# Kernel optimization log

Measured on AMD Instinct MI355X. Metric: run time of the kernel, lower is better.

The kernel has to match this reference:

```python
import jax, jax.numpy as jnp
import numpy as np

N_NODES = 100000
N_EDGES = 3200000
N_GRAPHS = 256
FEAT = 128
HIDDEN = 128
N_CLASSES = 10


def setup_inputs() -> dict:
    key = jax.random.key(0)
    ks = jax.random.split(key, 12)
    x = jax.random.normal(ks[0], (N_NODES, FEAT), dtype=jnp.float32)
    edge_index = jax.random.randint(ks[1], (2, N_EDGES), 0, N_NODES, dtype=jnp.int64)
    batch = jnp.sort(jax.random.randint(ks[2], (N_NODES,), 0, N_GRAPHS, dtype=jnp.int64))
    s = 0.05
    return {
        "x": x,
        "edge_index": edge_index,
        "batch": batch,
        "W1": jax.random.normal(ks[3], (FEAT, HIDDEN), dtype=jnp.float32) * s,
        "b1": jnp.zeros((HIDDEN,), dtype=jnp.float32),
        "W2": jax.random.normal(ks[4], (HIDDEN, HIDDEN), dtype=jnp.float32) * s,
        "b2": jnp.zeros((HIDDEN,), dtype=jnp.float32),
        "W3": jax.random.normal(ks[5], (HIDDEN, HIDDEN), dtype=jnp.float32) * s,
        "b3": jnp.zeros((HIDDEN,), dtype=jnp.float32),
        "lin1_w": jax.random.normal(ks[6], (HIDDEN, HIDDEN), dtype=jnp.float32) * s,
        "lin1_b": jnp.zeros((HIDDEN,), dtype=jnp.float32),
        "lin2_w": jax.random.normal(ks[7], (HIDDEN, N_CLASSES), dtype=jnp.float32) * s,
        "lin2_b": jnp.zeros((N_CLASSES,), dtype=jnp.float32),
    }


def _gcn_norm(edge_index, n_nodes):
    # PyG GCNConv default: add self-loops, symmetric normalization.
    src = jnp.concatenate([edge_index[0], jnp.arange(n_nodes, dtype=edge_index.dtype)])
    dst = jnp.concatenate([edge_index[1], jnp.arange(n_nodes, dtype=edge_index.dtype)])
    deg = jax.ops.segment_sum(jnp.ones_like(dst, dtype=jnp.float32), dst, num_segments=n_nodes)
    dis = jnp.where(deg > 0, jax.lax.rsqrt(jnp.maximum(deg, 1.0)), 0.0)
    norm = dis[src] * dis[dst]  # [E + N]
    return src, dst, norm


def _gcn_conv(x, src, dst, norm, W, b, n_nodes):
    h = x @ W                               # [N, H]
    msg = h[src] * norm[:, None]            # gather + scale, [E+N, H]
    out = jax.ops.segment_sum(msg, dst, num_segments=n_nodes)  # scatter-add
    return out + b


def reference(x, edge_index, batch, W1, b1, W2, b2, W3, b3, lin1_w, lin1_b, lin2_w, lin2_b):
    n = x.shape[0]
    src, dst, norm = _gcn_norm(edge_index, n)
    h = jax.nn.relu(_gcn_conv(x, src, dst, norm, W1, b1, n))
    h = jax.nn.relu(_gcn_conv(h, src, dst, norm, W2, b2, n))
    h = jax.nn.relu(_gcn_conv(h, src, dst, norm, W3, b3, n))
    # global mean pool over graphs
    sums = jax.ops.segment_sum(h, batch, num_segments=N_GRAPHS)
    cnts = jax.ops.segment_sum(jnp.ones((n,), dtype=h.dtype), batch, num_segments=N_GRAPHS)
    g = sums / jnp.maximum(cnts, 1.0)[:, None]
    g = jax.nn.relu(g @ lin1_w + lin1_b)
    # dropout p=0.5 is identity at inference
    return g @ lin2_w + lin2_b
```

## Files before the change

### kernel.cpp

```cpp
#include <hip/hip_runtime.h>
#include <hip/hip_fp16.h>

#define FEAT 128
#define CHUNK 8192
#define BSH 7
#define CAP 6144
#define RSTRIDE 784

#define QS  16.0f
#define QSI 0.0625f

typedef _Float16 half8 __attribute__((ext_vector_type(8)));
typedef float floatx4 __attribute__((ext_vector_type(4)));
typedef float floatx2 __attribute__((ext_vector_type(2)));

__device__ __forceinline__ unsigned int enc8x4(float a, float b, float c, float d) {
  unsigned int r = __builtin_amdgcn_cvt_pk_fp8_f32(a, b, 0u, false);
  return __builtin_amdgcn_cvt_pk_fp8_f32(c, d, r, true);
}
__device__ __forceinline__ void acc8(unsigned int w, float* a) {
  floatx2 v0 = __builtin_amdgcn_cvt_pk_f32_fp8(w, false);
  floatx2 v1 = __builtin_amdgcn_cvt_pk_f32_fp8(w, true);
  a[0] += v0.x; a[1] += v0.y; a[2] += v1.x; a[3] += v1.y;
}
__device__ __forceinline__ void acc8s(unsigned int w, float s, float* a) {
  floatx2 v0 = __builtin_amdgcn_cvt_pk_f32_fp8(w, false);
  floatx2 v1 = __builtin_amdgcn_cvt_pk_f32_fp8(w, true);
  a[0] = fmaf(s, v0.x, a[0]); a[1] = fmaf(s, v0.y, a[1]);
  a[2] = fmaf(s, v1.x, a[2]); a[3] = fmaf(s, v1.y, a[3]);
}


__global__ __launch_bounds__(256) void sort_prep_kernel(
    const int* __restrict__ ei, int E, int nchunks, int nbuk,
    int* __restrict__ pairs, int* __restrict__ runs,
    const float* __restrict__ W1, const float* __restrict__ W2,
    const float* __restrict__ W3, _Float16* __restrict__ P1,
    _Float16* __restrict__ P2, _Float16* __restrict__ P3,
    unsigned char* __restrict__ qA, unsigned char* __restrict__ qB,
    float* __restrict__ dis, float* __restrict__ gsum, int G, int N) {
  __shared__ int lhist[1024];
  __shared__ int lofs[1024];
  __shared__ int lcur[1024];
  __shared__ int tsum[256];
  __shared__ int stage[CHUNK];
  int t = threadIdx.x;
  if ((int)blockIdx.x >= nchunks) {
    int b = blockIdx.x - nchunks;
    if (b == 24) {
      if (t < 16) ((unsigned long long*)(qA + (size_t)N * FEAT))[t] = 0ull;
      else if (t < 32) ((unsigned long long*)(qB + (size_t)N * FEAT))[t - 16] = 0ull;
      else if (t == 32) dis[N] = 0.f;
      return;
    }
    if (b == 25) {
      float4 z = {0.f, 0.f, 0.f, 0.f};
      for (int i = t; i < G * 32; i += 256) ((float4*)gsum)[i] = z;
      return;
    }
    const float* W = (b < 8) ? W1 : (b < 16) ? W2 : W3;
    _Float16* P = (b < 8) ? P1 : (b < 16) ? P2 : P3;
    int e = (b & 7) * 256 + t;
    int l = e & 63;
    int ks = (e >> 6) & 3;
    int tn = e >> 8;
    int n = tn * 16 + (l & 15);
    int k0 = ks * 32 + (l >> 4) * 8;
    half8 v;
#pragma unroll
    for (int j = 0; j < 8; ++j) v[j] = (_Float16)W[(k0 + j) * 128 + n];
    *(half8*)(P + (size_t)e * 8) = v;
    return;
  }
  int c = blockIdx.x;
  int e0 = c * CHUNK;
  int e1 = e0 + CHUNK; if (e1 > E) e1 = E;
  int cnt = e1 - e0;
#pragma unroll
  for (int u = 0; u < 4; ++u) lhist[t + u * 256] = 0;
  __syncthreads();
  for (int j = e0 + t; j < e1; j += 256) atomicAdd(&lhist[ei[E + j] >> BSH], 1);
  __syncthreads();
  int a0 = lhist[4 * t], a1 = lhist[4 * t + 1];
  int a2 = lhist[4 * t + 2], a3 = lhist[4 * t + 3];
  int s = ((a0 + a1) + (a2 + a3));
  tsum[t] = s;
  __syncthreads();
  for (int o = 1; o < 256; o <<= 1) {
    int x = (t >= o) ? tsum[t - o] : 0;
    __syncthreads();
    tsum[t] += x;
    __syncthreads();
  }
  int base = tsum[t] - s;
  lofs[4 * t] = base;       lcur[4 * t] = base;
  lofs[4 * t + 1] = base + a0;           lcur[4 * t + 1] = base + a0;
  lofs[4 * t + 2] = base + a0 + a1;      lcur[4 * t + 2] = base + a0 + a1;
  lofs[4 * t + 3] = base + a0 + a1 + a2; lcur[4 * t + 3] = base + a0 + a1 + a2;
  __syncthreads();
  for (int k = t; k < nbuk; k += 256) runs[(size_t)c * RSTRIDE + k] = lofs[k];
  if (t == 0) runs[(size_t)c * RSTRIDE + nbuk] = cnt;
  for (int j = e0 + t; j < e1; j += 256) {
    int sv = ei[j];
    int d = ei[E + j];
    int p = atomicAdd(&lcur[d >> BSH], 1);
    stage[p] = sv | ((d & 127) << 24);
  }
  __syncthreads();
  for (int j = t; j < cnt; j += 256) pairs[e0 + j] = stage[j];
}

__global__ __launch_bounds__(256) void csr_mm1_kernel(
    const int* __restrict__ pairs, const int* __restrict__ runs, int nchunks,
    int nbuk, int2* __restrict__ row_se, float* __restrict__ dis,
    int* __restrict__ col,
    const float* __restrict__ Av, const _Float16* __restrict__ Wpk,
    unsigned char* __restrict__ qA, int N) {
  __shared__ int rs[512], rl[512], ro[512];
  __shared__ int cnt[128], sc[128];
  __shared__ int stage[CAP];
  int t = threadIdx.x;
  if ((int)blockIdx.x >= nbuk) {
    int wave = t >> 6, lane = t & 63;
    int quad = lane >> 4, nidx = lane & 15;
    int m0 = (blockIdx.x - nbuk) * 64 + wave * 16;
    int arow = m0 + nidx;
    bool avalid = arow < N;
    floatx4 acc[8];
#pragma unroll
    for (int tn = 0; tn < 8; ++tn) acc[tn] = (floatx4){0.f, 0.f, 0.f, 0.f};
#pragma unroll
    for (int ks = 0; ks < 4; ++ks) {
      half8 x = {};
      if (avalid) {
        const float* p = Av + (size_t)arow * 128 + ks * 32 + quad * 8;
        float4 f0 = *(const float4*)p;
        float4 f1 = *(const float4*)(p + 4);
        x[0] = (_Float16)f0.x; x[1] = (_Float16)f0.y;
        x[2] = (_Float16)f0.z; x[3] = (_Float16)f0.w;
        x[4] = (_Float16)f1.x; x[5] = (_Float16)f1.y;
        x[6] = (_Float16)f1.z; x[7] = (_Float16)f1.w;
      }
#pragma unroll
      for (int tn = 0; tn < 8; ++tn) {
        half8 wfrag = *(const half8*)(Wpk + ((size_t)((tn * 4 + ks) * 64 + lane)) * 8);
        acc[tn] = __builtin_amdgcn_mfma_f32_16x16x32_f16(wfrag, x, acc[tn], 0, 0, 0);
      }
    }
    if (avalid) {
#pragma unroll
      for (int tn = 0; tn < 8; ++tn) {
        unsigned int r = enc8x4(acc[tn][0] * QS, acc[tn][1] * QS,
                                acc[tn][2] * QS, acc[tn][3] * QS);
        *(unsigned int*)(qA + (size_t)arow * 128 + tn * 16 + quad * 4) = r;
      }
    }
    return;
  }
  int b = blockIdx.x;
  for (int c = t; c < 512; c += 256) {
    int s0 = 0, len = 0;
    if (c < nchunks) {
      const int* rr = runs + (size_t)c * RSTRIDE;
      s0 = rr[b];
      len = rr[b + 1] - s0;
    }
    rs[c] = s0; rl[c] = len;
  }
  if (t < 128) cnt[t] = 0;
  __syncthreads();
  ro[t] = rl[t]; ro[t + 256] = rl[t + 256];
  __syncthreads();
  for (int o = 1; o < 512; o <<= 1) {
    int v0 = (t >= o) ? ro[t - o] : 0;
    int v1 = (t + 256 >= o) ? ro[t + 256 - o] : 0;
    __syncthreads();
    ro[t] += v0; ro[t + 256] += v1;
    __syncthreads();
  }
  int ce = ro[511];
  int y0 = ro[t] - rl[t];
  int y1 = ro[t + 256] - rl[t + 256];
  __syncthreads();
  ro[t] = y0; ro[t + 256] = y1;
  __syncthreads();
  int colbase = b * CAP;
  bool fits = ce <= CAP;
  if (fits) {
    for (int c = t; c < nchunks; c += 256) {
      int gs = c * CHUNK + rs[c];
      int base = ro[c];
      int len = rl[c];
      for (int j = 0; j < len; ++j) {
        int p = pairs[gs + j];
        stage[base + j] = p;
        atomicAdd(&cnt[((unsigned)p) >> 24], 1);
      }
    }
  } else {
    for (int c = t; c < nchunks; c += 256) {
      int gs = c * CHUNK + rs[c];
      for (int j = 0; j < rl[c]; ++j)
        atomicAdd(&cnt[((unsigned)pairs[gs + j]) >> 24], 1);
    }
  }
  __syncthreads();
  int v = 0, excl = 0;
  if (t < 128) { v = cnt[t]; sc[t] = v; }
  __syncthreads();
  for (int o = 1; o < 128; o <<= 1) {
    int x = (t >= o && t < 128) ? sc[t - o] : 0;
    __syncthreads();
    if (t < 128) sc[t] += x;
    __syncthreads();
  }
  if (t < 128) {
    excl = sc[t] - v;
    int node = b * 128 + t;
    if (node < N) {
      row_se[node] = make_int2(colbase + excl, colbase + excl + v);
      dis[node] = rsqrtf((float)(v + 1));
    }
    cnt[t] = excl;
  }
  __syncthreads();
  if (fits) {
    for (int j = t; j < ce; j += 256) {
      int p = stage[j];
      int loc = atomicAdd(&cnt[((unsigned)p) >> 24], 1);
      col[colbase + loc] = (p & 0xFFFFFF) << 7;
    }
  } else {
    for (int c = t; c < nchunks; c += 256) {
      int gs = c * CHUNK + rs[c];
      for (int j = 0; j < rl[c]; ++j) {
        int p = pairs[gs + j];
        int loc = atomicAdd(&cnt[((unsigned)p) >> 24], 1);
        if (loc < CAP) col[colbase + loc] = (p & 0xFFFFFF) << 7;
      }
    }
  }
}


__global__ __launch_bounds__(256) void agg_fuse1_kernel(
    const unsigned char* __restrict__ hs_in, const int2* __restrict__ row_se,
    const int* __restrict__ col, const float* __restrict__ dis,
    const float* __restrict__ bias, const _Float16* __restrict__ Wpk,
    unsigned char* __restrict__ hs_out, int N) {
  __shared__ _Float16 Xs[32][136];
  int t = threadIdx.x;
  int wave = t >> 6, lane = t & 63;
  int lin = lane & 7;
  int nl = wave * 8 + (lane >> 3);
  int node = blockIdx.x * 32 + nl;
  bool valid = node < N;
  int lin16 = lin * 16;
  int zoff = N << 7;
  float a[16];
#pragma unroll
  for (int j = 0; j < 16; ++j) a[j] = 0.f;
  float ds = dis[valid ? node : N];
  int selfoff = (valid ? (node << 7) : zoff) + lin16;
  uint4 s0 = *(const uint4*)(hs_in + (unsigned)selfoff);
  acc8s(s0.x, ds, a); acc8s(s0.y, ds, a + 4);
  acc8s(s0.z, ds, a + 8); acc8s(s0.w, ds, a + 12);
  int2 se = valid ? row_se[node] : make_int2(0, 0);
  int i = se.x, e = se.y;
  while (__any(i < e)) {
    int c[8];
#pragma unroll
    for (int u = 0; u < 8; ++u) {
      int idx = i + u;
      c[u] = (idx < e) ? col[idx] : zoff;
    }
    uint4 r[8];
#pragma unroll
    for (int u = 0; u < 8; ++u)
      r[u] = *(const uint4*)(hs_in + (unsigned)(c[u] + lin16));
    float dv[8];
#pragma unroll
    for (int u = 0; u < 8; ++u) dv[u] = dis[(unsigned)c[u] >> 7];
#pragma unroll
    for (int u = 0; u < 8; ++u) {
      acc8s(r[u].x, dv[u], a);     acc8s(r[u].y, dv[u], a + 4);
      acc8s(r[u].z, dv[u], a + 8); acc8s(r[u].w, dv[u], a + 12);
    }
    i += 8;
  }
  float d = valid ? dis[node] * QSI : 0.f;
  const float* bp = bias + lin16;
  half8 hx0, hx1;
#pragma unroll
  for (int j = 0; j < 8; ++j) {
    float o0 = valid ? fmaxf(fmaf(d, a[j], bp[j]), 0.f) : 0.f;
    float o1 = valid ? fmaxf(fmaf(d, a[j + 8], bp[j + 8]), 0.f) : 0.f;
    hx0[j] = (_Float16)o0;
    hx1[j] = (_Float16)o1;
  }
  *(half8*)&Xs[nl][lin16] = hx0;
  *(half8*)&Xs[nl][lin16 + 8] = hx1;
  __syncthreads();
  int quad = lane >> 4, nidx = lane & 15;
  int ntile = wave >> 1;
  int f0 = (wave & 1) * 4;
  floatx4 acc[4];
#pragma unroll
  for (int f = 0; f < 4; ++f) acc[f] = (floatx4){0.f, 0.f, 0.f, 0.f};
#pragma unroll
  for (int ks = 0; ks < 4; ++ks) {
    half8 x = *(const half8*)&Xs[ntile * 16 + nidx][ks * 32 + quad * 8];
#pragma unroll
    for (int f = 0; f < 4; ++f) {
      half8 wf = *(const half8*)(Wpk + ((size_t)(((f0 + f) * 4 + ks) * 64 + lane)) * 8);
      acc[f] = __builtin_amdgcn_mfma_f32_16x16x32_f16(wf, x, acc[f], 0, 0, 0);
    }
  }
  int onode = blockIdx.x * 32 + ntile * 16 + nidx;
  if (onode < N) {
    float sc = dis[onode] * QS;
#pragma unroll
    for (int f = 0; f < 4; ++f) {
      unsigned int rq = enc8x4(acc[f][0] * sc, acc[f][1] * sc,
                               acc[f][2] * sc, acc[f][3] * sc);
      *(unsigned int*)(hs_out + (size_t)onode * 128 + (f0 + f) * 16 + quad * 4) = rq;
    }
  }
}

__global__ __launch_bounds__(256) void agg_fuse_kernel(
    const unsigned char* __restrict__ hs_in, const int2* __restrict__ row_se,
    const int* __restrict__ col, const float* __restrict__ dis,
    const float* __restrict__ bias, const _Float16* __restrict__ Wpk,
    unsigned char* __restrict__ hs_out, int N) {
  __shared__ _Float16 Xs[32][136];
  int t = threadIdx.x;
  int wave = t >> 6, lane = t & 63;
  int lin = lane & 7;
  int nl = wave * 8 + (lane >> 3);
  int node = blockIdx.x * 32 + nl;
  bool valid = node < N;
  int lin16 = lin * 16;
  int zoff = N << 7;
  float a[16];
#pragma unroll
  for (int j = 0; j < 16; ++j) a[j] = 0.f;
  int selfoff = (valid ? (node << 7) : zoff) + lin16;
  uint4 s0 = *(const uint4*)(hs_in + (unsigned)selfoff);
  acc8(s0.x, a); acc8(s0.y, a + 4); acc8(s0.z, a + 8); acc8(s0.w, a + 12);
  int2 se = valid ? row_se[node] : make_int2(0, 0);
  int i = se.x, e = se.y;
  while (__any(i < e)) {
    int c[8];
#pragma unroll
    for (int u = 0; u < 8; ++u) {
      int idx = i + u;
      c[u] = (idx < e) ? col[idx] : zoff;
    }
    uint4 r[8];
#pragma unroll
    for (int u = 0; u < 8; ++u)
      r[u] = *(const uint4*)(hs_in + (unsigned)(c[u] + lin16));
#pragma unroll
    for (int u = 0; u < 8; ++u) {
      acc8(r[u].x, a);     acc8(r[u].y, a + 4);
      acc8(r[u].z, a + 8); acc8(r[u].w, a + 12);
    }
    i += 8;
  }
  float d = valid ? dis[node] * QSI : 0.f;
  const float* bp = bias + lin16;
  half8 hx0, hx1;
#pragma unroll
  for (int j = 0; j < 8; ++j) {
    float o0 = valid ? fmaxf(fmaf(d, a[j], bp[j]), 0.f) : 0.f;
    float o1 = valid ? fmaxf(fmaf(d, a[j + 8], bp[j + 8]), 0.f) : 0.f;
    hx0[j] = (_Float16)o0;
    hx1[j] = (_Float16)o1;
  }
  *(half8*)&Xs[nl][lin16] = hx0;
  *(half8*)&Xs[nl][lin16 + 8] = hx1;
  __syncthreads();
  int quad = lane >> 4, nidx = lane & 15;
  int ntile = wave >> 1;
  int f0 = (wave & 1) * 4;
  floatx4 acc[4];
#pragma unroll
  for (int f = 0; f < 4; ++f) acc[f] = (floatx4){0.f, 0.f, 0.f, 0.f};
#pragma unroll
  for (int ks = 0; ks < 4; ++ks) {
    half8 x = *(const half8*)&Xs[ntile * 16 + nidx][ks * 32 + quad * 8];
#pragma unroll
    for (int f = 0; f < 4; ++f) {
      half8 wf = *(const half8*)(Wpk + ((size_t)(((f0 + f) * 4 + ks) * 64 + lane)) * 8);
      acc[f] = __builtin_amdgcn_mfma_f32_16x16x32_f16(wf, x, acc[f], 0, 0, 0);
    }
  }
  int onode = blockIdx.x * 32 + ntile * 16 + nidx;
  if (onode < N) {
    float sc = dis[onode] * QS;
#pragma unroll
    for (int f = 0; f < 4; ++f) {
      unsigned int rq = enc8x4(acc[f][0] * sc, acc[f][1] * sc,
                               acc[f][2] * sc, acc[f][3] * sc);
      *(unsigned int*)(hs_out + (size_t)onode * 128 + (f0 + f) * 16 + quad * 4) = rq;
    }
  }
}

__global__ __launch_bounds__(256) void agg_pool_kernel(
    const unsigned char* __restrict__ hs, const int2* __restrict__ row_se,
    const int* __restrict__ col, const float* __restrict__ dis,
    const float* __restrict__ bias, const int* __restrict__ batch,
    float* __restrict__ gsum, int N) {
  __shared__ float Hs[32][132];
  __shared__ int ig[32];
  int t = threadIdx.x;
  int wave = t >> 6, lane = t & 63;
  int lin = lane & 7;
  int nl = wave * 8 + (lane >> 3);
  int node = blockIdx.x * 32 + nl;
  bool valid = node < N;
  int lin16 = lin * 16;
  int zoff = N << 7;
  float a[16];
#pragma unroll
  for (int j = 0; j < 16; ++j) a[j] = 0.f;
  int selfoff = (valid ? (node << 7) : zoff) + lin16;
  uint4 s0 = *(const uint4*)(hs + (unsigned)selfoff);
  acc8(s0.x, a); acc8(s0.y, a + 4); acc8(s0.z, a + 8); acc8(s0.w, a + 12);
  int2 se = valid ? row_se[node] : make_int2(0, 0);
  int i = se.x, e = se.y;
  while (__any(i < e)) {
    int c[8];
#pragma unroll
    for (int u = 0; u < 8; ++u) {
      int idx = i + u;
      c[u] = (idx < e) ? col[idx] : zoff;
    }
    uint4 r[8];
#pragma unroll
    for (int u = 0; u < 8; ++u)
      r[u] = *(const uint4*)(hs + (unsigned)(c[u] + lin16));
#pragma unroll
    for (int u = 0; u < 8; ++u) {
      acc8(r[u].x, a);     acc8(r[u].y, a + 4);
      acc8(r[u].z, a + 8); acc8(r[u].w, a + 12);
    }
    i += 8;
  }
  float d = valid ? dis[node] * QSI : 0.f;
  const float* bp = bias + lin16;
#pragma unroll
  for (int j = 0; j < 16; ++j)
    Hs[nl][lin16 + j] = valid ? fmaxf(fmaf(d, a[j], bp[j]), 0.f) : 0.f;
  if (lin == 0) ig[nl] = batch[valid ? node : (N - 1)];
  __syncthreads();
  if (t < 128) {
    float run = 0.f;
    int cur = ig[0];
#pragma unroll 4
    for (int n = 0; n < 32; ++n) {
      int g2 = ig[n];
      if (g2 != cur) {
        atomicAdd(&gsum[cur * 128 + t], run);
        run = 0.f;
        cur = g2;
      }
      run += Hs[n][t];
    }
    atomicAdd(&gsum[cur * 128 + t], run);
  }
}

__global__ __launch_bounds__(128) void head_kernel(
    const float* __restrict__ gsum, const int* __restrict__ batch,
    const float* __restrict__ l1w, const float* __restrict__ l1b,
    const float* __restrict__ l2w, const float* __restrict__ l2b,
    float* __restrict__ out, int N, int C) {
  __shared__ float row[128];
  __shared__ float row2[128];
  int grp = blockIdx.x, t = threadIdx.x;
  int lo = 0, hi = N;
  while (lo < hi) { int m = (lo + hi) >> 1; if (batch[m] < grp) lo = m + 1; else hi = m; }
  int start = lo;
  hi = N;
  while (lo < hi) { int m = (lo + hi) >> 1; if (batch[m] <= grp) lo = m + 1; else hi = m; }
  int end = lo;
  float cntf = (float)(end - start);
  row[t] = gsum[grp * 128 + t] / fmaxf(cntf, 1.0f);
  __syncthreads();
  float acc = l1b[t];
#pragma unroll 8
  for (int k = 0; k < 128; ++k) acc = fmaf(row[k], l1w[k * 128 + t], acc);
  row2[t] = fmaxf(acc, 0.f);
  __syncthreads();
  if (t < C) {
    float a = l2b[t];
#pragma unroll 8
    for (int k = 0; k < 128; ++k) a = fmaf(row2[k], l2w[k * C + t], a);
    out[grp * C + t] = a;
  }
}


extern "C" void kernel_launch(void* const* d_in, const int* in_sizes, int n_in,
                              void* d_out, int out_size, void* d_ws, size_t ws_size,
                              hipStream_t stream) {
  const float* x   = (const float*)d_in[0];
  const int*   ei  = (const int*)d_in[1];
  const int*   bat = (const int*)d_in[2];
  const float* W1  = (const float*)d_in[3];
  const float* b1  = (const float*)d_in[4];
  const float* W2  = (const float*)d_in[5];
  const float* b2  = (const float*)d_in[6];
  const float* W3  = (const float*)d_in[7];
  const float* b3  = (const float*)d_in[8];
  const float* l1w = (const float*)d_in[9];
  const float* l1b = (const float*)d_in[10];
  const float* l2w = (const float*)d_in[11];
  const float* l2b = (const float*)d_in[12];

  int N = in_sizes[2];
  int E = in_sizes[1] / 2;
  int C = in_sizes[12];
  int G = out_size / C;
  float* outp = (float*)d_out;

  char* wp = (char*)d_ws;
  auto alloc = [&](size_t bytes) -> void* {
    void* p = (void*)wp;
    wp += (bytes + 255) & ~(size_t)255;
    return p;
  };
  int nbuk    = (N + 127) / 128;
  int nchunks = (E + CHUNK - 1) / CHUNK;
  int mmB     = (N + 63) / 64;

  float*    dis    = (float*)alloc((size_t)(N + 1) * 4);
  int2*     row_se = (int2*)alloc((size_t)N * 8);
  int*      col    = (int*)alloc((size_t)nbuk * CAP * 4);
  int*      pairs  = (int*)alloc((size_t)nchunks * CHUNK * 4);
  int*      runs   = (int*)alloc((size_t)nchunks * RSTRIDE * 4);
  _Float16* Wpk1   = (_Float16*)alloc(16384 * 2);
  _Float16* Wpk2   = (_Float16*)alloc(16384 * 2);
  _Float16* Wpk3   = (_Float16*)alloc(16384 * 2);
  unsigned char* qA = (unsigned char*)alloc((size_t)(N + 1) * FEAT);
  unsigned char* qB = (unsigned char*)alloc((size_t)(N + 1) * FEAT);
  float*    gsum   = (float*)alloc((size_t)G * FEAT * 4);

  sort_prep_kernel<<<nchunks + 26, 256, 0, stream>>>(
      ei, E, nchunks, nbuk, pairs, runs, W1, W2, W3, Wpk1, Wpk2, Wpk3,
      qA, qB, dis, gsum, G, N);
  csr_mm1_kernel<<<nbuk + mmB, 256, 0, stream>>>(pairs, runs, nchunks, nbuk,
                                                 row_se, dis, col,
                                                 x, Wpk1, qA, N);

  int gB = (N + 31) / 32;
  agg_fuse1_kernel<<<gB, 256, 0, stream>>>(qA, row_se, col, dis, b1,
                                           Wpk2, qB, N);
  agg_fuse_kernel<<<gB, 256, 0, stream>>>(qB, row_se, col, dis, b2,
                                          Wpk3, qA, N);
  agg_pool_kernel<<<gB, 256, 0, stream>>>(qA, row_se, col, dis, b3, bat,
                                          gsum, N);
  head_kernel<<<G, 128, 0, stream>>>(gsum, bat, l1w, l1b, l2w, l2b, outp, N, C);
}
```

Before: 432.5 us.

## Move first-layer GEMM into sort kernel with per-block LDS weight packing

```diff
diff --git a/kernel.cpp b/kernel.cpp
--- a/kernel.cpp
+++ b/kernel.cpp
@@ -30,14 +30,14 @@
   a[2] = fmaf(s, v1.x, a[2]); a[3] = fmaf(s, v1.y, a[3]);
 }
 
-
-__global__ __launch_bounds__(256) void sort_prep_kernel(
+__global__ __launch_bounds__(256) void sort_prep_mm1_kernel(
     const int* __restrict__ ei, int E, int nchunks, int nbuk,
     int* __restrict__ pairs, int* __restrict__ runs,
     const float* __restrict__ W1, const float* __restrict__ W2,
-    const float* __restrict__ W3, _Float16* __restrict__ P1,
-    _Float16* __restrict__ P2, _Float16* __restrict__ P3,
-    unsigned char* __restrict__ qA, unsigned char* __restrict__ qB,
+    const float* __restrict__ W3, _Float16* __restrict__ P2,
+    _Float16* __restrict__ P3,
+    const float* __restrict__ Av, unsigned char* __restrict__ qA,
+    unsigned char* __restrict__ qB,
     float* __restrict__ dis, float* __restrict__ gsum, int G, int N) {
   __shared__ int lhist[1024];
   __shared__ int lofs[1024];
@@ -47,83 +47,48 @@
   int t = threadIdx.x;
   if ((int)blockIdx.x >= nchunks) {
     int b = blockIdx.x - nchunks;
-    if (b == 24) {
+    if (b < 16) {
+      const float* W = (b < 8) ? W2 : W3;
+      _Float16* P = (b < 8) ? P2 : P3;
+      int e = (b & 7) * 256 + t;
+      int l = e & 63;
+      int ks = (e >> 6) & 3;
+      int tn = e >> 8;
+      int n = tn * 16 + (l & 15);
+      int k0 = ks * 32 + (l >> 4) * 8;
+      half8 v;
+#pragma unroll
+      for (int j = 0; j < 8; ++j) v[j] = (_Float16)W[(k0 + j) * 128 + n];
+      *(half8*)(P + (size_t)e * 8) = v;
+      return;
+    }
+    if (b == 16) {
       if (t < 16) ((unsigned long long*)(qA + (size_t)N * FEAT))[t] = 0ull;
       else if (t < 32) ((unsigned long long*)(qB + (size_t)N * FEAT))[t - 16] = 0ull;
       else if (t == 32) dis[N] = 0.f;
       return;
     }
-    if (b == 25) {
+    if (b == 17) {
       float4 z = {0.f, 0.f, 0.f, 0.f};
       for (int i = t; i < G * 32; i += 256) ((float4*)gsum)[i] = z;
       return;
     }
-    const float* W = (b < 8) ? W1 : (b < 16) ? W2 : W3;
-    _Float16* P = (b < 8) ? P1 : (b < 16) ? P2 : P3;
-    int e = (b & 7) * 256 + t;
-    int l = e & 63;
-    int ks = (e >> 6) & 3;
-    int tn = e >> 8;
-    int n = tn * 16 + (l & 15);
-    int k0 = ks * 32 + (l >> 4) * 8;
-    half8 v;
-#pragma unroll
-    for (int j = 0; j < 8; ++j) v[j] = (_Float16)W[(k0 + j) * 128 + n];
-    *(half8*)(P + (size_t)e * 8) = v;
-    return;
-  }
-  int c = blockIdx.x;
-  int e0 = c * CHUNK;
-  int e1 = e0 + CHUNK; if (e1 > E) e1 = E;
-  int cnt = e1 - e0;
-#pragma unroll
-  for (int u = 0; u < 4; ++u) lhist[t + u * 256] = 0;
-  __syncthreads();
-  for (int j = e0 + t; j < e1; j += 256) atomicAdd(&lhist[ei[E + j] >> BSH], 1);
-  __syncthreads();
-  int a0 = lhist[4 * t], a1 = lhist[4 * t + 1];
-  int a2 = lhist[4 * t + 2], a3 = lhist[4 * t + 3];
-  int s = ((a0 + a1) + (a2 + a3));
-  tsum[t] = s;
-  __syncthreads();
-  for (int o = 1; o < 256; o <<= 1) {
-    int x = (t >= o) ? tsum[t - o] : 0;
-    __syncthreads();
-    tsum[t] += x;
-    __syncthreads();
-  }
-  int base = tsum[t] - s;
-  lofs[4 * t] = base;       lcur[4 * t] = base;
-  lofs[4 * t + 1] = base + a0;           lcur[4 * t + 1] = base + a0;
-  lofs[4 * t + 2] = base + a0 + a1;      lcur[4 * t + 2] = base + a0 + a1;
-  lofs[4 * t + 3] = base + a0 + a1 + a2; lcur[4 * t + 3] = base + a0 + a1 + a2;
-  __syncthreads();
-  for (int k = t; k < nbuk; k += 256) runs[(size_t)c * RSTRIDE + k] = lofs[k];
-  if (t == 0) runs[(size_t)c * RSTRIDE + nbuk] = cnt;
-  for (int j = e0 + t; j < e1; j += 256) {
-    int sv = ei[j];
-    int d = ei[E + j];
-    int p = atomicAdd(&lcur[d >> BSH], 1);
-    stage[p] = sv | ((d & 127) << 24);
-  }
-  __syncthreads();
-  for (int j = t; j < cnt; j += 256) pairs[e0 + j] = stage[j];
-}
-
-__global__ __launch_bounds__(256) void csr_mm1_kernel(
-    const int* __restrict__ pairs, const int* __restrict__ runs, int nchunks,
-    int nbuk, int2* __restrict__ row_se, float* __restrict__ dis,
-    int* __restrict__ col,
-    const float* __restrict__ Av, const _Float16* __restrict__ Wpk,
-    unsigned char* __restrict__ qA, int N) {
-  __shared__ int rs[512], rl[512], ro[512];
-  __shared__ int cnt[128], sc[128];
-  __shared__ int stage[CAP];
-  int t = threadIdx.x;
-  if ((int)blockIdx.x >= nbuk) {
+    _Float16* Wl = (_Float16*)stage;
+    for (int e = t; e < 2048; e += 256) {
+      int l = e & 63;
+      int ks = (e >> 6) & 3;
+      int tn = e >> 8;
+      int n = tn * 16 + (l & 15);
+      int k0 = ks * 32 + (l >> 4) * 8;
+      half8 v;
+#pragma unroll
+      for (int j = 0; j < 8; ++j) v[j] = (_Float16)W1[(k0 + j) * 128 + n];
+      *(half8*)(Wl + (size_t)e * 8) = v;
+    }
+    __syncthreads();
     int wave = t >> 6, lane = t & 63;
     int quad = lane >> 4, nidx = lane & 15;
-    int m0 = (blockIdx.x - nbuk) * 64 + wave * 16;
+    int m0 = (b - 18) * 64 + wave * 16;
     int arow = m0 + nidx;
     bool avalid = arow < N;
     floatx4 acc[8];
@@ -143,7 +108,7 @@
       }
 #pragma unroll
       for (int tn = 0; tn < 8; ++tn) {
-        half8 wfrag = *(const half8*)(Wpk + ((size_t)((tn * 4 + ks) * 64 + lane)) * 8);
+        half8 wfrag = *(const half8*)(Wl + ((size_t)((tn * 4 + ks) * 64 + lane)) * 8);
         acc[tn] = __builtin_amdgcn_mfma_f32_16x16x32_f16(wfrag, x, acc[tn], 0, 0, 0);
       }
     }
@@ -157,7 +122,52 @@
     }
     return;
   }
-  int b = blockIdx.x;
+  int c = blockIdx.x;
+  int e0 = c * CHUNK;
+  int e1 = e0 + CHUNK; if (e1 > E) e1 = E;
+  int cnt = e1 - e0;
+#pragma unroll
+  for (int u = 0; u < 4; ++u) lhist[t + u * 256] = 0;
+  __syncthreads();
+  for (int j = e0 + t; j < e1; j += 256) atomicAdd(&lhist[ei[E + j] >> BSH], 1);
+  __syncthreads();
+  int a0 = lhist[4 * t], a1 = lhist[4 * t + 1];
+  int a2 = lhist[4 * t + 2], a3 = lhist[4 * t + 3];
+  int s = ((a0 + a1) + (a2 + a3));
+  tsum[t] = s;
+  __syncthreads();
+  for (int o = 1; o < 256; o <<= 1) {
+    int x = (t >= o) ? tsum[t - o] : 0;
+    __syncthreads();
+    tsum[t] += x;
+    __syncthreads();
+  }
+  int base = tsum[t] - s;
+  lofs[4 * t] = base;       lcur[4 * t] = base;
+  lofs[4 * t + 1] = base + a0;           lcur[4 * t + 1] = base + a0;
+  lofs[4 * t + 2] = base + a0 + a1;      lcur[4 * t + 2] = base + a0 + a1;
+  lofs[4 * t + 3] = base + a0 + a1 + a2; lcur[4 * t + 3] = base + a0 + a1 + a2;
+  __syncthreads();
+  for (int k = t; k < nbuk; k += 256) runs[(size_t)c * RSTRIDE + k] = lofs[k];
+  if (t == 0) runs[(size_t)c * RSTRIDE + nbuk] = cnt;
+  for (int j = e0 + t; j < e1; j += 256) {
+    int sv = ei[j];
+    int d = ei[E + j];
+    int p = atomicAdd(&lcur[d >> BSH], 1);
+    stage[p] = sv | ((d & 127) << 24);
+  }
+  __syncthreads();
+  for (int j = t; j < cnt; j += 256) pairs[e0 + j] = stage[j];
+}
+
+__global__ __launch_bounds__(256) void bucket_csr_kernel(
+    const int* __restrict__ pairs, const int* __restrict__ runs, int nchunks,
+    int nbuk, int2* __restrict__ row_se, float* __restrict__ dis,
+    int* __restrict__ col, int N) {
+  __shared__ int rs[512], rl[512], ro[512];
+  __shared__ int cnt[128], sc[128];
+  __shared__ int stage[CAP];
+  int b = blockIdx.x, t = threadIdx.x;
   for (int c = t; c < 512; c += 256) {
     int s0 = 0, len = 0;
     if (c < nchunks) {
@@ -542,19 +552,17 @@
   int*      col    = (int*)alloc((size_t)nbuk * CAP * 4);
   int*      pairs  = (int*)alloc((size_t)nchunks * CHUNK * 4);
   int*      runs   = (int*)alloc((size_t)nchunks * RSTRIDE * 4);
-  _Float16* Wpk1   = (_Float16*)alloc(16384 * 2);
   _Float16* Wpk2   = (_Float16*)alloc(16384 * 2);
   _Float16* Wpk3   = (_Float16*)alloc(16384 * 2);
   unsigned char* qA = (unsigned char*)alloc((size_t)(N + 1) * FEAT);
   unsigned char* qB = (unsigned char*)alloc((size_t)(N + 1) * FEAT);
   float*    gsum   = (float*)alloc((size_t)G * FEAT * 4);
 
-  sort_prep_kernel<<<nchunks + 26, 256, 0, stream>>>(
-      ei, E, nchunks, nbuk, pairs, runs, W1, W2, W3, Wpk1, Wpk2, Wpk3,
-      qA, qB, dis, gsum, G, N);
-  csr_mm1_kernel<<<nbuk + mmB, 256, 0, stream>>>(pairs, runs, nchunks, nbuk,
-                                                 row_se, dis, col,
-                                                 x, Wpk1, qA, N);
+  sort_prep_mm1_kernel<<<nchunks + 18 + mmB, 256, 0, stream>>>(
+      ei, E, nchunks, nbuk, pairs, runs, W1, W2, W3, Wpk2, Wpk3,
+      x, qA, qB, dis, gsum, G, N);
+  bucket_csr_kernel<<<nbuk, 256, 0, stream>>>(pairs, runs, nchunks, nbuk,
+                                              row_se, dis, col, N);
 
   int gB = (N + 31) / 32;
   agg_fuse1_kernel<<<gB, 256, 0, stream>>>(qA, row_se, col, dis, b1,
```

After: 433.1 us. No clear change (+0.1%).
